# Performance work log

Hardware: AMD Instinct MI355X
Metric: run time of the kernel (lower is better)

The kernel has to match this reference:

```python
import jax, jax.numpy as jnp
import numpy as np

B, S, F = 4, 4096, 128
GAMMA = 0.96875


def setup_inputs() -> dict:
    key = jax.random.key(0)
    ks = jax.random.split(key, 8)
    x = jax.random.normal(ks[0], (B, S, F), dtype=jnp.float32)
    # torch nn.Linear params: W [out,in], b [out]
    lim = 1.0 / np.sqrt(F)
    Wq = jax.random.uniform(ks[1], (F, F), jnp.float32, -lim, lim)
    bq = jax.random.uniform(ks[2], (F,), jnp.float32, -lim, lim)
    Wk = jax.random.uniform(ks[3], (F, F), jnp.float32, -lim, lim)
    bk = jax.random.uniform(ks[4], (F,), jnp.float32, -lim, lim)
    Wv = jax.random.uniform(ks[5], (F, F), jnp.float32, -lim, lim)
    bv = jax.random.uniform(ks[6], (F,), jnp.float32, -lim, lim)
    theta = jax.random.uniform(ks[7], (1, F), jnp.float32)  # th.rand
    return {"x": x, "Wq": Wq, "bq": bq, "Wk": Wk, "bk": bk, "Wv": Wv, "bv": bv, "theta": theta}


def _masks(Sn, theta, dtype):
    # rotary-like phase: index [S,1] @ theta [1,F] -> [S,F]
    idx = jnp.arange(1, Sn + 1, dtype=dtype)[:, None]
    mt = idx * theta  # broadcasted outer product, [S,F]
    cos, sin = jnp.cos(mt), jnp.sin(mt)
    # causal exponential decay mask: gamma**(i-j) for i>=j else 0
    i = jnp.arange(Sn)[:, None]
    j = jnp.arange(Sn)[None, :]
    e = i - j
    decay = jnp.where(e >= 0, jnp.asarray(GAMMA, dtype) ** jnp.maximum(e, 0).astype(dtype), jnp.asarray(0.0, dtype))
    return cos, sin, decay


def reference(x, Wq, bq, Wk, bk, Wv, bv, theta):
    Bn, Sn, Fn = x.shape
    q = x @ Wq.T + bq
    k = x @ Wk.T + bk
    v = x @ Wv.T + bv
    cos, sin, decay = _masks(Sn, theta, x.dtype)
    # retention scores: QK^T under cos/sin modulation, [B,S,S]
    scores = jnp.einsum('bsf,btf->bst', q * cos, k * cos) \
           + jnp.einsum('bsf,btf->bst', q * sin, k * sin)
    scores = scores * decay
    return jnp.einsum('bst,btf->bsf', scores, v)
```

## Files before the change

kernel.cpp:

```cpp
#include <hip/hip_runtime.h>


#define S_LEN 4096
#define B_N   4
#define F_N   128
#define WIN   512
#define LOG2_GAMMA (-0.0458036905705339f)

typedef unsigned short u16;
typedef unsigned int   u32;
typedef __attribute__((ext_vector_type(8))) short bf16x8;
typedef __attribute__((ext_vector_type(4))) float f32x4;

__device__ inline u16 f2bf(float x) {
    u32 u = __builtin_bit_cast(u32, x);
    u32 r = (u + 0x7fffu + ((u >> 16) & 1u)) >> 16;
    return (u16)r;
}

__device__ inline uint4 pack8(const u16* p) {
    uint4 v;
    v.x = (u32)p[0] | ((u32)p[1] << 16);
    v.y = (u32)p[2] | ((u32)p[3] << 16);
    v.z = (u32)p[4] | ((u32)p[5] << 16);
    v.w = (u32)p[6] | ((u32)p[7] << 16);
    return v;
}

__global__ void prep_kernel(const float* __restrict__ Wq,
                            const float* __restrict__ Wk,
                            const float* __restrict__ Wv,
                            u16* __restrict__ WbF)
{
    const int idx    = blockIdx.x * 256 + threadIdx.x;
    const int lane   = idx & 63;
    const int fragid = idx >> 6;
    const int ks     = fragid & 3;
    const int nt     = (fragid >> 2) & 7;
    const int mat    = fragid >> 5;
    const float* W = (mat == 0) ? Wq : (mat == 1 ? Wk : Wv);
    const float* src = W + (nt * 16 + (lane & 15)) * F_N + ks * 32 + (lane >> 4) * 8;
    float4 a = *(const float4*)src;
    float4 b = *(const float4*)(src + 4);
    u16 o[8] = {f2bf(a.x), f2bf(a.y), f2bf(a.z), f2bf(a.w),
                f2bf(b.x), f2bf(b.y), f2bf(b.z), f2bf(b.w)};
    *(uint4*)(WbF + fragid * 512 + lane * 8) = pack8(o);
}

__global__ __launch_bounds__(256, 2)
void proj_kernel(const float* __restrict__ x, const u16* __restrict__ WbF,
                 const float* __restrict__ bq, const float* __restrict__ bk,
                 const float* __restrict__ bv, const float* __restrict__ theta,
                 u16* __restrict__ QbF, u16* __restrict__ Kb,
                 u16* __restrict__ VtF)
{
    __shared__ __align__(16) u16 xb[32 * 136];
    __shared__ __align__(16) u16 obuf[32 * 264];

    const int tid  = threadIdx.x;
    const int lane = tid & 63;
    const int w    = __builtin_amdgcn_readfirstlane(tid >> 6);
    const int r0   = blockIdx.x * 32;
    const int b    = r0 >> 12;
    const int s0   = r0 & (S_LEN - 1);
    const int col  = lane & 15;
    const int quad = lane >> 4;
    const int mt   = w & 1;
    const int nh   = w >> 1;

#pragma unroll
    for (int it = 0; it < 4; ++it) {
        const int c   = it * 256 + tid;
        const int row = c >> 5;
        const int k0  = (c & 31) * 4;
        float4 v = *(const float4*)(x + (r0 + row) * F_N + k0);
        u16 o[4] = {f2bf(v.x), f2bf(v.y), f2bf(v.z), f2bf(v.w)};
        *(uint2*)(xb + row * 136 + k0) =
            make_uint2((u32)o[0] | ((u32)o[1] << 16), (u32)o[2] | ((u32)o[3] << 16));
    }
    __syncthreads();

    bf16x8 af[4];
#pragma unroll
    for (int ks = 0; ks < 4; ++ks)
        af[ks] = *(const bf16x8*)(xb + (mt * 16 + col) * 136 + ks * 32 + quad * 8);

    f32x4 qa[4], ka[4], va[4];
#pragma unroll
    for (int nt = 0; nt < 4; ++nt) {
        qa[nt] = (f32x4){0.f, 0.f, 0.f, 0.f};
        ka[nt] = (f32x4){0.f, 0.f, 0.f, 0.f};
        va[nt] = (f32x4){0.f, 0.f, 0.f, 0.f};
    }
#pragma unroll
    for (int nt = 0; nt < 4; ++nt) {
        const int ng = nh * 4 + nt;
#pragma unroll
        for (int ks = 0; ks < 4; ++ks) {
            bf16x8 bqf = *(const bf16x8*)(WbF + ((0 * 8 + ng) * 4 + ks) * 512 + lane * 8);
            bf16x8 bkf = *(const bf16x8*)(WbF + ((1 * 8 + ng) * 4 + ks) * 512 + lane * 8);
            bf16x8 bvf = *(const bf16x8*)(WbF + ((2 * 8 + ng) * 4 + ks) * 512 + lane * 8);
            qa[nt] = __builtin_amdgcn_mfma_f32_16x16x32_bf16(af[ks], bqf, qa[nt], 0, 0, 0);
            ka[nt] = __builtin_amdgcn_mfma_f32_16x16x32_bf16(af[ks], bkf, ka[nt], 0, 0, 0);
            va[nt] = __builtin_amdgcn_mfma_f32_16x16x32_bf16(af[ks], bvf, va[nt], 0, 0, 0);
        }
    }

    float bqv[4], bkv[4], bvv[4], thv[4];
#pragma unroll
    for (int nt = 0; nt < 4; ++nt) {
        const int o = nh * 64 + nt * 16 + col;
        bqv[nt] = bq[o]; bkv[nt] = bk[o]; bvv[nt] = bv[o]; thv[nt] = theta[o];
    }
    float cs[16], sn[16];
#pragma unroll
    for (int nt = 0; nt < 4; ++nt)
#pragma unroll
        for (int r = 0; r < 4; ++r) {
            const int srow = s0 + mt * 16 + quad * 4 + r;
            __sincosf((float)(srow + 1) * thv[nt], &sn[nt * 4 + r], &cs[nt * 4 + r]);
        }

#pragma unroll
    for (int nt = 0; nt < 4; ++nt)
#pragma unroll
        for (int r = 0; r < 4; ++r) {
            const float q = qa[nt][r] + bqv[nt];
            const int row = mt * 16 + quad * 4 + r;
            const int o   = nh * 64 + nt * 16 + col;
            obuf[row * 264 + o]       = f2bf(q * cs[nt * 4 + r]);
            obuf[row * 264 + 128 + o] = f2bf(q * sn[nt * 4 + r]);
        }
    __syncthreads();
#pragma unroll
    for (int it = 0; it < 4; ++it) {
        const int c  = it * 256 + tid;
        const int gl = c >> 9;
        const int ks = (c >> 6) & 7;
        const int ln = c & 63;
        uint4 v = *(const uint4*)(obuf + (gl * 16 + (ln & 15)) * 264 +
                                  ks * 32 + (ln >> 4) * 8);
        *(uint4*)(QbF + (((b * 256 + (s0 >> 4) + gl) * 8 + ks) * 512) + ln * 8) = v;
    }
    __syncthreads();

#pragma unroll
    for (int nt = 0; nt < 4; ++nt)
#pragma unroll
        for (int r = 0; r < 4; ++r) {
            const float k = ka[nt][r] + bkv[nt];
            const int row = mt * 16 + quad * 4 + r;
            const int o   = nh * 64 + nt * 16 + col;
            obuf[row * 264 + o]       = f2bf(k * cs[nt * 4 + r]);
            obuf[row * 264 + 128 + o] = f2bf(k * sn[nt * 4 + r]);
        }
    __syncthreads();
#pragma unroll
    for (int it = 0; it < 4; ++it) {
        const int c   = it * 256 + tid;
        const int row = c >> 5;
        const int k0  = (c & 31) * 8;
        uint4 v = *(const uint4*)(obuf + row * 264 + k0);
        *(uint4*)(Kb + (r0 + row) * 256 + k0) = v;
    }
    __syncthreads();

#pragma unroll
    for (int nt = 0; nt < 4; ++nt)
#pragma unroll
        for (int r = 0; r < 4; ++r) {
            const float vv = va[nt][r] + bvv[nt];
            const int f  = nh * 64 + nt * 16 + col;
            const int sl = mt * 16 + quad * 4 + r;
            obuf[f * 40 + sl] = f2bf(vv);
        }
    __syncthreads();
#pragma unroll
    for (int it = 0; it < 2; ++it) {
        const int c  = it * 256 + tid;
        const int ft = c >> 6;
        const int ln = c & 63;
        uint4 v = *(const uint4*)(obuf + (ft * 16 + (ln & 15)) * 40 + (ln >> 4) * 8);
        *(uint4*)(VtF + ((b * 128 + (s0 >> 5)) * 8 + ft) * 512 + ln * 8) = v;
    }
}

__global__ __launch_bounds__(256, 2)
void retention_kernel(const u16* __restrict__ QbF, const u16* __restrict__ Kb,
                      const u16* __restrict__ VtF, float* __restrict__ out)
{
    __shared__ __align__(16) u16 K_lds[64 * 264];
    __shared__ __align__(16) u16 P_lds[32 * 136];

    const int tid  = threadIdx.x;
    const int lane = tid & 63;
    const int w    = __builtin_amdgcn_readfirstlane(tid >> 6);
    const int b    = blockIdx.y;
    const int s0   = blockIdx.x * 32;
    const int col  = lane & 15;
    const int quad = lane >> 4;
    const int ssub = (w & 1) * 16;
    const int fh   = w >> 1;

    const int t_start = (s0 >= WIN) ? ((s0 - WIN) & ~63) : 0;
    const int nch     = (s0 + 32 - t_start + 63) >> 6;

    const u16* Kbb = Kb + (b << 12) * 256;

    const int g = ((s0 + ssub) >> 4);
    bf16x8 qf[8];
#pragma unroll
    for (int ks = 0; ks < 8; ++ks)
        qf[ks] = *(const bf16x8*)(QbF + ((b * 256 + g) * 8 + ks) * 512 + lane * 8);

    f32x4 oacc[4];
#pragma unroll
    for (int ft = 0; ft < 4; ++ft) oacc[ft] = (f32x4){0.f, 0.f, 0.f, 0.f};

    for (int ch = 0; ch < nch; ++ch) {
        const int tc = t_start + (ch << 6);
#pragma unroll
        for (int i = 0; i < 8; ++i) {
            const int c  = i * 256 + tid;
            const int t  = c >> 5;
            const int k0 = (c & 31) * 8;
            int trow = tc + t; if (trow > S_LEN - 1) trow = S_LEN - 1;
            uint4 v = *(const uint4*)(Kbb + trow * 256 + k0);
            *(uint4*)(K_lds + t * 264 + k0) = v;
        }
        __syncthreads();

#pragma unroll
        for (int tp = 0; tp < 2; ++tp) {
            const int tt = fh * 2 + tp;
            f32x4 acc = (f32x4){0.f, 0.f, 0.f, 0.f};
#pragma unroll
            for (int ks = 0; ks < 8; ++ks) {
                bf16x8 bfr = *(const bf16x8*)(K_lds + (tt * 16 + col) * 264 +
                                              ks * 32 + quad * 8);
                acc = __builtin_amdgcn_mfma_f32_16x16x32_bf16(qf[ks], bfr, acc, 0, 0, 0);
            }
            const int tglob = tc + tt * 16 + col;
#pragma unroll
            for (int r = 0; r < 4; ++r) {
                const int sglob = s0 + ssub + quad * 4 + r;
                const int e = sglob - tglob;
                const float d = (e >= 0) ? exp2f((float)e * LOG2_GAMMA) : 0.f;
                P_lds[(ssub + quad * 4 + r) * 136 + tt * 16 + col] = f2bf(acc[r] * d);
            }
        }
        __syncthreads();

        bf16x8 pa[2];
#pragma unroll
        for (int ks = 0; ks < 2; ++ks)
            pa[ks] = *(const bf16x8*)(P_lds + (ssub + col) * 136 + ks * 32 + quad * 8);
#pragma unroll
        for (int ks = 0; ks < 2; ++ks) {
            int tb = (tc >> 5) + ks; if (tb > 127) tb = 127;
#pragma unroll
            for (int ft = 0; ft < 4; ++ft) {
                const int ftg = fh * 4 + ft;
                bf16x8 vb = *(const bf16x8*)(VtF + ((b * 128 + tb) * 8 + ftg) * 512 +
                                             lane * 8);
                oacc[ft] = __builtin_amdgcn_mfma_f32_16x16x32_bf16(pa[ks], vb,
                                                                   oacc[ft], 0, 0, 0);
            }
        }
    }

    float* ob = out + ((b << 12) + s0) * F_N;
#pragma unroll
    for (int ft = 0; ft < 4; ++ft)
#pragma unroll
        for (int r = 0; r < 4; ++r)
            ob[(ssub + quad * 4 + r) * F_N + fh * 64 + ft * 16 + col] = oacc[ft][r];
}

extern "C" void kernel_launch(void* const* d_in, const int* in_sizes, int n_in,
                              void* d_out, int out_size, void* d_ws, size_t ws_size,
                              hipStream_t stream) {
    const float* x     = (const float*)d_in[0];
    const float* Wq    = (const float*)d_in[1];
    const float* bq    = (const float*)d_in[2];
    const float* Wk    = (const float*)d_in[3];
    const float* bk    = (const float*)d_in[4];
    const float* Wv    = (const float*)d_in[5];
    const float* bv    = (const float*)d_in[6];
    const float* theta = (const float*)d_in[7];
    float* out = (float*)d_out;

    u16* ws  = (u16*)d_ws;
    u16* QbF = ws;
    u16* Kb  = ws + 4194304;
    u16* VtF = ws + 8388608;
    u16* WbF = ws + 10485760;

    prep_kernel<<<24, 256, 0, stream>>>(Wq, Wk, Wv, WbF);
    proj_kernel<<<512, 256, 0, stream>>>(x, WbF, bq, bk, bv, theta, QbF, Kb, VtF);
    retention_kernel<<<dim3(128, B_N), 256, 0, stream>>>(QbF, Kb, VtF, out);
}
```

Before: 116.5 us.

## Double-buffer K chunks via async global-to-LDS loads with swizzled layout

The retention kernel now stages K chunks into a double-buffered LDS region using global_load_lds, prefetching the next chunk while the current one is computed. The K layout is XOR-swizzled, written that way by the projection kernel, so no LDS padding is needed, and V fragments are loaded into registers early. The projection kernel writes Q and K to separate LDS buffers to remove two barriers, and the retention blocks are remapped in interleaved order to balance work. The risks are the hand-written vmcnt/lgkmcnt waits and higher LDS and register use, which could lower occupancy.

Result: faster. 105.2 us (-9.7%).

```diff
diff --git a/kernel.cpp b/kernel.cpp
--- a/kernel.cpp
+++ b/kernel.cpp
@@ -55,7 +55,8 @@
                  u16* __restrict__ VtF)
 {
     __shared__ __align__(16) u16 xb[32 * 136];
-    __shared__ __align__(16) u16 obuf[32 * 264];
+    __shared__ __align__(16) u16 obufQ[32 * 264];
+    __shared__ __align__(16) u16 obufK[32 * 264];
 
     const int tid  = threadIdx.x;
     const int lane = tid & 63;
@@ -126,42 +127,34 @@
 #pragma unroll
         for (int r = 0; r < 4; ++r) {
             const float q = qa[nt][r] + bqv[nt];
+            const float k = ka[nt][r] + bkv[nt];
             const int row = mt * 16 + quad * 4 + r;
             const int o   = nh * 64 + nt * 16 + col;
-            obuf[row * 264 + o]       = f2bf(q * cs[nt * 4 + r]);
-            obuf[row * 264 + 128 + o] = f2bf(q * sn[nt * 4 + r]);
+            const float c = cs[nt * 4 + r], s = sn[nt * 4 + r];
+            obufQ[row * 264 + o]       = f2bf(q * c);
+            obufQ[row * 264 + 128 + o] = f2bf(q * s);
+            obufK[row * 264 + o]       = f2bf(k * c);
+            obufK[row * 264 + 128 + o] = f2bf(k * s);
         }
     __syncthreads();
+
 #pragma unroll
     for (int it = 0; it < 4; ++it) {
         const int c  = it * 256 + tid;
         const int gl = c >> 9;
         const int ks = (c >> 6) & 7;
         const int ln = c & 63;
-        uint4 v = *(const uint4*)(obuf + (gl * 16 + (ln & 15)) * 264 +
+        uint4 v = *(const uint4*)(obufQ + (gl * 16 + (ln & 15)) * 264 +
                                   ks * 32 + (ln >> 4) * 8);
         *(uint4*)(QbF + (((b * 256 + (s0 >> 4) + gl) * 8 + ks) * 512) + ln * 8) = v;
     }
-    __syncthreads();
-
-#pragma unroll
-    for (int nt = 0; nt < 4; ++nt)
-#pragma unroll
-        for (int r = 0; r < 4; ++r) {
-            const float k = ka[nt][r] + bkv[nt];
-            const int row = mt * 16 + quad * 4 + r;
-            const int o   = nh * 64 + nt * 16 + col;
-            obuf[row * 264 + o]       = f2bf(k * cs[nt * 4 + r]);
-            obuf[row * 264 + 128 + o] = f2bf(k * sn[nt * 4 + r]);
-        }
-    __syncthreads();
 #pragma unroll
     for (int it = 0; it < 4; ++it) {
         const int c   = it * 256 + tid;
         const int row = c >> 5;
-        const int k0  = (c & 31) * 8;
-        uint4 v = *(const uint4*)(obuf + row * 264 + k0);
-        *(uint4*)(Kb + (r0 + row) * 256 + k0) = v;
+        const int k4  = c & 31;
+        uint4 v = *(const uint4*)(obufK + row * 264 + k4 * 8);
+        *(uint4*)(Kb + (r0 + row) * 256 + ((k4 ^ (row & 7)) * 8)) = v;
     }
     __syncthreads();
 
@@ -172,7 +165,7 @@
             const float vv = va[nt][r] + bvv[nt];
             const int f  = nh * 64 + nt * 16 + col;
             const int sl = mt * 16 + quad * 4 + r;
-            obuf[f * 40 + sl] = f2bf(vv);
+            obufQ[f * 40 + sl] = f2bf(vv);
         }
     __syncthreads();
 #pragma unroll
@@ -180,7 +173,7 @@
         const int c  = it * 256 + tid;
         const int ft = c >> 6;
         const int ln = c & 63;
-        uint4 v = *(const uint4*)(obuf + (ft * 16 + (ln & 15)) * 40 + (ln >> 4) * 8);
+        uint4 v = *(const uint4*)(obufQ + (ft * 16 + (ln & 15)) * 40 + (ln >> 4) * 8);
         *(uint4*)(VtF + ((b * 128 + (s0 >> 5)) * 8 + ft) * 512 + ln * 8) = v;
     }
 }
@@ -189,14 +182,16 @@
 void retention_kernel(const u16* __restrict__ QbF, const u16* __restrict__ Kb,
                       const u16* __restrict__ VtF, float* __restrict__ out)
 {
-    __shared__ __align__(16) u16 K_lds[64 * 264];
+    __shared__ __align__(16) u16 K_lds[2 * 64 * 256];
     __shared__ __align__(16) u16 P_lds[32 * 136];
 
     const int tid  = threadIdx.x;
     const int lane = tid & 63;
     const int w    = __builtin_amdgcn_readfirstlane(tid >> 6);
     const int b    = blockIdx.y;
-    const int s0   = blockIdx.x * 32;
+    const int bx   = blockIdx.x;
+    const int sblk = ((bx & 7) << 4) + (bx >> 3);
+    const int s0   = sblk * 32;
     const int col  = lane & 15;
     const int quad = lane >> 4;
     const int ssub = (w & 1) * 16;
@@ -205,7 +200,7 @@
     const int t_start = (s0 >= WIN) ? ((s0 - WIN) & ~63) : 0;
     const int nch     = (s0 + 32 - t_start + 63) >> 6;
 
-    const u16* Kbb = Kb + (b << 12) * 256;
+    const char* KbbC = (const char*)(Kb + (b << 12) * 256);
 
     const int g = ((s0 + ssub) >> 4);
     bf16x8 qf[8];
@@ -217,30 +212,53 @@
 #pragma unroll
     for (int ft = 0; ft < 4; ++ft) oacc[ft] = (f32x4){0.f, 0.f, 0.f, 0.f};
 
+    auto stage = [&](int tcs, int buf) {
+#pragma unroll
+        for (int i = 0; i < 8; ++i) {
+            const int m   = i * 4 + w;
+            const int row = m * 2 + (lane >> 5);
+            int trow = tcs + row; if (trow > S_LEN - 1) trow = S_LEN - 1;
+            const char* gp = KbbC + trow * 512 + (lane & 31) * 16;
+            char* lp = (char*)K_lds + buf * 32768 + m * 1024;
+            __builtin_amdgcn_global_load_lds(
+                (const __attribute__((address_space(1))) u32*)gp,
+                (__attribute__((address_space(3))) u32*)lp, 16, 0, 0);
+        }
+    };
+
+    stage(t_start, 0);
+
     for (int ch = 0; ch < nch; ++ch) {
-        const int tc = t_start + (ch << 6);
-#pragma unroll
-        for (int i = 0; i < 8; ++i) {
-            const int c  = i * 256 + tid;
-            const int t  = c >> 5;
-            const int k0 = (c & 31) * 8;
-            int trow = tc + t; if (trow > S_LEN - 1) trow = S_LEN - 1;
-            uint4 v = *(const uint4*)(Kbb + trow * 256 + k0);
-            *(uint4*)(K_lds + t * 264 + k0) = v;
-        }
-        __syncthreads();
+        const int tc  = t_start + (ch << 6);
+        const int cur = ch & 1;
+
+        bf16x8 vbr[8];
+#pragma unroll
+        for (int ks = 0; ks < 2; ++ks) {
+            int tb = (tc >> 5) + ks; if (tb > 127) tb = 127;
+#pragma unroll
+            for (int ft = 0; ft < 4; ++ft)
+                vbr[ks * 4 + ft] = *(const bf16x8*)(VtF +
+                    ((b * 128 + tb) * 8 + fh * 4 + ft) * 512 + lane * 8);
+        }
+
+        stage(tc + 64, cur ^ 1);
+
+        asm volatile("s_waitcnt vmcnt(16)" ::: "memory");
+        __builtin_amdgcn_s_barrier();
 
 #pragma unroll
         for (int tp = 0; tp < 2; ++tp) {
             const int tt = fh * 2 + tp;
+            const int t  = tt * 16 + col;
             f32x4 acc = (f32x4){0.f, 0.f, 0.f, 0.f};
 #pragma unroll
             for (int ks = 0; ks < 8; ++ks) {
-                bf16x8 bfr = *(const bf16x8*)(K_lds + (tt * 16 + col) * 264 +
-                                              ks * 32 + quad * 8);
+                const int blk = (ks * 4 + quad) ^ (col & 7);
+                bf16x8 bfr = *(const bf16x8*)(K_lds + cur * 16384 + t * 256 + blk * 8);
                 acc = __builtin_amdgcn_mfma_f32_16x16x32_bf16(qf[ks], bfr, acc, 0, 0, 0);
             }
-            const int tglob = tc + tt * 16 + col;
+            const int tglob = tc + t;
 #pragma unroll
             for (int r = 0; r < 4; ++r) {
                 const int sglob = s0 + ssub + quad * 4 + r;
@@ -249,24 +267,19 @@
                 P_lds[(ssub + quad * 4 + r) * 136 + tt * 16 + col] = f2bf(acc[r] * d);
             }
         }
-        __syncthreads();
+        asm volatile("s_waitcnt lgkmcnt(0)" ::: "memory");
+        __builtin_amdgcn_s_barrier();
 
         bf16x8 pa[2];
 #pragma unroll
         for (int ks = 0; ks < 2; ++ks)
             pa[ks] = *(const bf16x8*)(P_lds + (ssub + col) * 136 + ks * 32 + quad * 8);
 #pragma unroll
-        for (int ks = 0; ks < 2; ++ks) {
-            int tb = (tc >> 5) + ks; if (tb > 127) tb = 127;
-#pragma unroll
-            for (int ft = 0; ft < 4; ++ft) {
-                const int ftg = fh * 4 + ft;
-                bf16x8 vb = *(const bf16x8*)(VtF + ((b * 128 + tb) * 8 + ftg) * 512 +
-                                             lane * 8);
-                oacc[ft] = __builtin_amdgcn_mfma_f32_16x16x32_bf16(pa[ks], vb,
-                                                                   oacc[ft], 0, 0, 0);
-            }
-        }
+        for (int ks = 0; ks < 2; ++ks)
+#pragma unroll
+            for (int ft = 0; ft < 4; ++ft)
+                oacc[ft] = __builtin_amdgcn_mfma_f32_16x16x32_bf16(pa[ks],
+                                vbr[ks * 4 + ft], oacc[ft], 0, 0, 0);
     }
 
     float* ob = out + ((b << 12) + s0) * F_N;
```
